# Kernel tuning notes

Hardware: AMD Instinct MI355X
Metric: run time of the kernel (lower is better)

## Reference

```python
import jax, jax.numpy as jnp
import numpy as np

N, D_IN = 16384, 1024
E, K = 16, 2
D_EMB, H_UNITS, D_HID = 128, 1024, 512


def setup_inputs() -> dict:
    key = jax.random.key(0)
    ks = jax.random.split(key, 10)
    s = lambda fan_in: 1.0 / np.sqrt(fan_in)
    return {
        "x": jax.random.normal(ks[0], (N, D_IN), jnp.float32),
        "Wr": jax.random.normal(ks[1], (D_IN, D_EMB), jnp.float32) * s(D_IN),
        "br": jnp.zeros((D_EMB,), jnp.float32),
        "expert_embeddings": jax.random.normal(ks[2], (E, D_EMB), jnp.float32) * s(D_EMB),
        "W1": jax.random.normal(ks[3], (E, D_IN, H_UNITS), jnp.float32) * s(D_IN),
        "b1": jnp.zeros((E, H_UNITS), jnp.float32),
        "W2": jax.random.normal(ks[4], (E, H_UNITS, H_UNITS // 2), jnp.float32) * s(H_UNITS),
        "b2": jnp.zeros((E, H_UNITS // 2), jnp.float32),
        "W3": jax.random.normal(ks[5], (E, H_UNITS // 2, D_HID), jnp.float32) * s(H_UNITS // 2),
        "b3": jnp.zeros((E, D_HID), jnp.float32),
    }


def reference(x, Wr, br, expert_embeddings, W1, b1, W2, b2, W3, b3):
    # Router: query per token [N, D_EMB]
    q = x @ Wr + br
    # Negative squared L2 distance to each expert embedding -> scores [N, E]
    d2 = jnp.sum(jnp.square(q[:, None, :] - expert_embeddings[None, :, :]), axis=-1)
    scores = -d2
    # Top-k gating (softmax over the k selected scores only)
    top_k_scores, top_k_idx = jax.lax.top_k(scores, K)        # [N, K]
    gates = jax.nn.softmax(top_k_scores, axis=-1)             # [N, K]
    # Dense all-expert MLP (as the original: every expert on every token)
    h1 = jax.nn.relu(jnp.einsum('nd,edh->enh', x, W1) + b1[:, None, :])   # [E,N,1024]
    h2 = jax.nn.relu(jnp.einsum('enh,ehm->enm', h1, W2) + b2[:, None, :]) # [E,N,512]
    eo = jnp.einsum('enm,emo->eno', h2, W3) + b3[:, None, :]              # [E,N,D_HID]
    eo_t = jnp.transpose(eo, (1, 0, 2))                                   # [N,E,D_HID]
    # Gather top-k expert outputs per token and combine with gates
    sel = jnp.take_along_axis(eo_t, top_k_idx[:, :, None], axis=1)        # [N,K,D_HID]
    combined = jnp.sum(sel * gates[:, :, None], axis=1)                   # [N,D_HID]
    return combined
```

## Files before the change

### kernel.cpp

```cpp
#include <hip/hip_runtime.h>

typedef unsigned short u16;
typedef __attribute__((ext_vector_type(8))) short short8;
typedef __attribute__((ext_vector_type(4))) float f32x4;

#define N_TOK 16384
#define DIN   1024
#define NE    16
#define DEMB  128
#define H1N   1024
#define H2N   512
#define DOUT  512
#define CAP   34816
#define MT    (CAP/128)
#define RBLK  1024

#define OFF_P      0ul
#define OFF_C      65536ul
#define OFF_CTRL   65792ul
#define OFF_E01    66048ul
#define OFF_G01    197120ul
#define OFF_GTOK   328192ul
#define OFF_GGATE  467456ul
#define OFF_BH     606720ul
#define OFF_BB     672256ul
#define OFF_W1T    737792ul
#define OFF_W2T    34292224ul
#define OFF_W3T    51069440ul
#define OFF_XBF    59458048ul
#define OFF_H1     93012480ul
#define OFF_H2     164315648ul

__device__ __forceinline__ u16 f2bf(float f) {
  union { float f; unsigned u; } v; v.f = f;
  unsigned r = v.u + 0x7fff + ((v.u >> 16) & 1);
  return (u16)(r >> 16);
}

__device__ __forceinline__ void async_copy16(const u16* g, u16* l) {
  __builtin_amdgcn_global_load_lds((const __attribute__((address_space(1))) unsigned*)g,
                                   (__attribute__((address_space(3))) unsigned*)l,
                                   16, 0, 0);
}

__global__ void router_prep(const float* __restrict__ Wr, const float* __restrict__ br,
                            const float* __restrict__ emb, float* __restrict__ P,
                            float* __restrict__ c) {
  int idx = blockIdx.x * 256 + threadIdx.x;
  int row = idx >> 4, e = idx & 15;
  float s = 0.f;
  for (int j = 0; j < DEMB; ++j) s += Wr[row * DEMB + j] * emb[e * DEMB + j];
  P[row * NE + e] = 2.f * s;
  if (idx < NE) {
    float cc = 0.f, n2 = 0.f;
    for (int j = 0; j < DEMB; ++j) {
      float ev = emb[idx * DEMB + j];
      cc += br[j] * ev;
      n2 += ev * ev;
    }
    c[idx] = 2.f * cc - n2;
  }
}

__global__ void __launch_bounds__(256) router_score(
    const float* __restrict__ x, const float* __restrict__ P,
    const float* __restrict__ c, int* __restrict__ e01,
    float* __restrict__ g01, int* __restrict__ bhist,
    u16* __restrict__ xbf) {
  __shared__ float xs[16384];
  __shared__ int lh[16];
  int wave = threadIdx.x >> 6, lane = threadIdx.x & 63;
  int e2 = lane & 7, kgl = lane >> 3;
  int tbase = blockIdx.x * 16 + wave * 4;
  float* xw = xs + wave * 4096;

  if (threadIdx.x < 16) lh[threadIdx.x] = 0;

  u16* xbrow = xbf + (size_t)tbase * DIN;
  #pragma unroll
  for (int t = 0; t < 4; ++t) {
    const float* src = x + (size_t)(tbase + t) * DIN;
    #pragma unroll
    for (int q = 0; q < 4; ++q) {
      int g = q * 256 + lane * 4;
      float4 v = *(const float4*)(src + g);
      *(float4*)(xw + t * 1024 + g) = v;
      ushort4 o;
      o.x = f2bf(v.x); o.y = f2bf(v.y); o.z = f2bf(v.z); o.w = f2bf(v.w);
      *(ushort4*)(xbrow + t * DIN + g) = o;
    }
  }
  __syncthreads();

  int te0 = 2 * e2, te1 = te0 + 1;
  float ce0 = c[te0], ce1 = c[te1];
  const float* Pb = P + te0;

  float acc0[4] = {0.f, 0.f, 0.f, 0.f};
  float acc1[4] = {0.f, 0.f, 0.f, 0.f};
  int cbase = kgl * 128;
  #pragma unroll 4
  for (int i = 0; i < 32; ++i) {
    int w = (kgl * 4 + i * 4) & 127;
    int idx = cbase + w;
    float2 pv0 = *(const float2*)(Pb + (size_t)(idx + 0) * NE);
    float2 pv1 = *(const float2*)(Pb + (size_t)(idx + 1) * NE);
    float2 pv2 = *(const float2*)(Pb + (size_t)(idx + 2) * NE);
    float2 pv3 = *(const float2*)(Pb + (size_t)(idx + 3) * NE);
    #pragma unroll
    for (int t = 0; t < 4; ++t) {
      float4 xv = *(const float4*)(xw + t * 1024 + idx);
      acc0[t] = fmaf(xv.x, pv0.x, acc0[t]); acc1[t] = fmaf(xv.x, pv0.y, acc1[t]);
      acc0[t] = fmaf(xv.y, pv1.x, acc0[t]); acc1[t] = fmaf(xv.y, pv1.y, acc1[t]);
      acc0[t] = fmaf(xv.z, pv2.x, acc0[t]); acc1[t] = fmaf(xv.z, pv2.y, acc1[t]);
      acc0[t] = fmaf(xv.w, pv3.x, acc0[t]); acc1[t] = fmaf(xv.w, pv3.y, acc1[t]);
    }
  }

  for (int t = 0; t < 4; ++t) {
    float s0 = acc0[t], s1 = acc1[t];
    #pragma unroll
    for (int off = 8; off <= 32; off <<= 1) {
      s0 += __shfl_xor(s0, off);
      s1 += __shfl_xor(s1, off);
    }
    s0 += ce0; s1 += ce1;
    float hi; int hidx;
    if (s0 >= s1) { hi = s0; hidx = te0; } else { hi = s1; hidx = te1; }
    float m1 = hi; int i1 = hidx;
    #pragma unroll
    for (int off = 1; off < 8; off <<= 1) {
      float so = __shfl_xor(m1, off); int io = __shfl_xor(i1, off);
      if (so > m1 || (so == m1 && io < i1)) { m1 = so; i1 = io; }
    }
    float c2; int c2i;
    if (i1 == te0)      { c2 = s1; c2i = te1; }
    else if (i1 == te1) { c2 = s0; c2i = te0; }
    else                { c2 = hi; c2i = hidx; }
    float m2 = c2; int i2 = c2i;
    #pragma unroll
    for (int off = 1; off < 8; off <<= 1) {
      float so = __shfl_xor(m2, off); int io = __shfl_xor(i2, off);
      if (so > m2 || (so == m2 && io < i2)) { m2 = so; i2 = io; }
    }
    if (lane == 0) {
      int tok = tbase + t;
      float ev = expf(m2 - m1);
      float inv = 1.f / (1.f + ev);
      e01[tok * 2 + 0] = i1; e01[tok * 2 + 1] = i2;
      g01[tok * 2 + 0] = inv; g01[tok * 2 + 1] = ev * inv;
      atomicAdd(&lh[i1], 1);
      atomicAdd(&lh[i2], 1);
    }
  }
  __syncthreads();
  if (threadIdx.x < 16) bhist[blockIdx.x * 16 + threadIdx.x] = lh[threadIdx.x];
}

__global__ void __launch_bounds__(1024) scan_offsets(
    const int* __restrict__ bhist, int* __restrict__ counts,
    int* __restrict__ poff, int* __restrict__ bbase, int* __restrict__ gtok) {
  int t = threadIdx.x;
  int e = t & 15, ch = t >> 4;
  int b0 = ch * 16;
  int s = 0;
  #pragma unroll
  for (int i = 0; i < 16; ++i) s += bhist[(b0 + i) * 16 + e];
  __shared__ int part[64][16];
  __shared__ int chbase[64][16];
  __shared__ int cnt[16];
  __shared__ int pof[16];
  part[ch][e] = s;
  __syncthreads();
  if (t < 16) {
    int run = 0;
    for (int c2 = 0; c2 < 64; ++c2) { chbase[c2][t] = run; run += part[c2][t]; }
    cnt[t] = run;
  }
  __syncthreads();
  if (t == 0) {
    int off = 0;
    for (int e2 = 0; e2 < NE; ++e2) {
      pof[e2] = off;
      poff[e2] = off;
      counts[e2] = cnt[e2];
      off += (cnt[e2] + 127) & ~127;
    }
    poff[NE] = off;
  }
  __syncthreads();
  int padc = ((cnt[e] + 127) & ~127) - cnt[e];
  int pbase = pof[e] + cnt[e];
  if (ch < padc) gtok[pbase + ch] = 0;
  if (ch + 64 < padc) gtok[pbase + ch + 64] = 0;

  int run = pof[e] + chbase[ch][e];
  #pragma unroll
  for (int i = 0; i < 16; ++i) {
    bbase[(b0 + i) * 16 + e] = run;
    run += bhist[(b0 + i) * 16 + e];
  }
}

__global__ void build_lists(const int* __restrict__ e01, const float* __restrict__ g01,
                            const int* __restrict__ bbase, int* __restrict__ gtok,
                            float* __restrict__ ggate) {
  __shared__ int pos[16];
  int tid = threadIdx.x;
  if (tid < 16) pos[tid] = bbase[blockIdx.x * 16 + tid];
  __syncthreads();
  if (tid < 16) {
    int t = blockIdx.x * 16 + tid;
    #pragma unroll
    for (int k = 0; k < 2; ++k) {
      int e = e01[t * 2 + k];
      int p = atomicAdd(&pos[e], 1);
      gtok[p] = t;
      ggate[p] = g01[t * 2 + k];
    }
  }
}

template<int K, int N>
__global__ void conv_w(const float* __restrict__ W, u16* __restrict__ WT) {
  __shared__ float tile[64][65];
  int e = blockIdx.z;
  int n0 = blockIdx.x * 64, k0 = blockIdx.y * 64;
  int tx = threadIdx.x & 63, ty = threadIdx.x >> 6;
  const float* Wb = W + (size_t)e * K * N;
  #pragma unroll
  for (int p = 0; p < 16; ++p) {
    int k = p * 4 + ty;
    tile[k][tx] = Wb[(size_t)(k0 + k) * N + n0 + tx];
  }
  __syncthreads();
  u16* WTb = WT + (size_t)e * N * K;
  #pragma unroll
  for (int p = 0; p < 16; ++p) {
    int n = p * 4 + ty;
    WTb[(size_t)(n0 + n) * K + k0 + tx] = f2bf(tile[tx][n]);
  }
}

template<int MODE, bool INDIR>
__global__ void __launch_bounds__(256)
gemm_moe(const u16* __restrict__ A, const u16* __restrict__ Ball,
         const float* __restrict__ bias, u16* __restrict__ Cb, float* __restrict__ outF,
         const int* __restrict__ poff, const int* __restrict__ counts,
         const int* __restrict__ gtok, const float* __restrict__ ggate,
         int K, int N, int nblk) {
  __shared__ u16 Asm[2][4096];
  __shared__ u16 Bsm[2][4096];

  int bid = blockIdx.x;
  int q = nblk >> 3, r = nblk & 7;
  int xcd = bid & 7, sidx = bid >> 3;
  int wg = (xcd < r ? xcd * (q + 1) : r * (q + 1) + (xcd - r) * q) + sidx;
  int NB = N >> 7;
  int rb = wg / NB, nb = wg - rb * NB;

  int row_base = rb * 128;
  if (row_base >= poff[NE]) return;
  int e = 0;
  while (row_base >= poff[e + 1]) ++e;

  int tid = threadIdx.x;
  int wave = tid >> 6, lane = tid & 63;
  int wm = wave >> 1, wn = wave & 1;
  int fr = lane & 15, kq = lane >> 4;
  int n_base = nb * 128;

  const u16* Brow = Ball + (size_t)e * N * K + (size_t)n_base * K;

  int rr0 = tid >> 2, rr1 = rr0 + 64;
  int ch8 = ((tid & 3) ^ ((rr0 >> 1) & 3)) * 8;
  const u16 *a0, *a1;
  if constexpr (INDIR) {
    a0 = A + (size_t)gtok[row_base + rr0] * K;
    a1 = A + (size_t)gtok[row_base + rr1] * K;
  } else {
    a0 = A + (size_t)(row_base + rr0) * K;
    a1 = A + (size_t)(row_base + rr1) * K;
  }
  const u16* b0 = Brow + (size_t)rr0 * K;
  const u16* b1 = Brow + (size_t)rr1 * K;

  f32x4 acc[4][4];
  #pragma unroll
  for (int m = 0; m < 4; ++m)
    #pragma unroll
    for (int n = 0; n < 4; ++n)
      acc[m][n] = (f32x4){0.f, 0.f, 0.f, 0.f};

  int swz = (fr >> 1) & 3;

  auto stage_tile = [&](int buf, int kt) {
    async_copy16(a0 + kt + ch8, &Asm[buf][tid * 8]);
    async_copy16(a1 + kt + ch8, &Asm[buf][(256 + tid) * 8]);
    async_copy16(b0 + kt + ch8, &Bsm[buf][tid * 8]);
    async_copy16(b1 + kt + ch8, &Bsm[buf][(256 + tid) * 8]);
  };

  stage_tile(0, 0);
  __syncthreads();

  int nstep = K >> 5;
  int cur = 0;
  for (int s = 0; s < nstep; ++s) {
    if (s + 1 < nstep) stage_tile(cur ^ 1, (s + 1) << 5);
    short8 av[4], bv[4];
    #pragma unroll
    for (int m = 0; m < 4; ++m)
      av[m] = *(const short8*)(&Asm[cur][((wm * 64 + m * 16 + fr) * 4 + (kq ^ swz)) * 8]);
    #pragma unroll
    for (int n = 0; n < 4; ++n)
      bv[n] = *(const short8*)(&Bsm[cur][((wn * 64 + n * 16 + fr) * 4 + (kq ^ swz)) * 8]);
    #pragma unroll
    for (int m = 0; m < 4; ++m)
      #pragma unroll
      for (int n = 0; n < 4; ++n)
        acc[m][n] = __builtin_amdgcn_mfma_f32_16x16x32_bf16(av[m], bv[n], acc[m][n], 0, 0, 0);
    __syncthreads();
    cur ^= 1;
  }

  int crow = (lane >> 4) * 4;
  int ccol = lane & 15;
  const float* be = bias + (size_t)e * N;
  if constexpr (MODE == 0) {
    #pragma unroll
    for (int m = 0; m < 4; ++m) {
      int gr0 = row_base + wm * 64 + m * 16 + crow;
      #pragma unroll
      for (int n = 0; n < 4; ++n) {
        int gc = n_base + wn * 64 + n * 16 + ccol;
        float bvs = be[gc];
        #pragma unroll
        for (int r2 = 0; r2 < 4; ++r2) {
          float v = acc[m][n][r2] + bvs;
          v = v > 0.f ? v : 0.f;
          Cb[(size_t)(gr0 + r2) * N + gc] = f2bf(v);
        }
      }
    }
  } else {
    int poe = poff[e], ce = counts[e];
    #pragma unroll
    for (int m = 0; m < 4; ++m) {
      int gr0 = row_base + wm * 64 + m * 16 + crow;
      int tk[4]; float gt[4]; bool vl[4];
      #pragma unroll
      for (int r2 = 0; r2 < 4; ++r2) {
        int gr = gr0 + r2;
        vl[r2] = (gr - poe) < ce;
        tk[r2] = vl[r2] ? gtok[gr] : 0;
        gt[r2] = vl[r2] ? ggate[gr] : 0.f;
      }
      #pragma unroll
      for (int n = 0; n < 4; ++n) {
        int gc = n_base + wn * 64 + n * 16 + ccol;
        float bvs = be[gc];
        #pragma unroll
        for (int r2 = 0; r2 < 4; ++r2) {
          if (vl[r2]) {
            float v = (acc[m][n][r2] + bvs) * gt[r2];
            atomicAdd(outF + (size_t)tk[r2] * N + gc, v);
          }
        }
      }
    }
  }
}

extern "C" void kernel_launch(void* const* d_in, const int* in_sizes, int n_in,
                              void* d_out, int out_size, void* d_ws, size_t ws_size,
                              hipStream_t stream) {
  const float* x   = (const float*)d_in[0];
  const float* Wr  = (const float*)d_in[1];
  const float* br  = (const float*)d_in[2];
  const float* emb = (const float*)d_in[3];
  const float* W1  = (const float*)d_in[4];
  const float* b1  = (const float*)d_in[5];
  const float* W2  = (const float*)d_in[6];
  const float* b2  = (const float*)d_in[7];
  const float* W3  = (const float*)d_in[8];
  const float* b3  = (const float*)d_in[9];
  float* out = (float*)d_out;
  char* ws = (char*)d_ws;

  float* P      = (float*)(ws + OFF_P);
  float* c      = (float*)(ws + OFF_C);
  int*   counts = (int*)(ws + OFF_CTRL);
  int*   poff   = (int*)(ws + OFF_CTRL + 128);
  int*   e01    = (int*)(ws + OFF_E01);
  float* g01    = (float*)(ws + OFF_G01);
  int*   gtok   = (int*)(ws + OFF_GTOK);
  float* ggate  = (float*)(ws + OFF_GGATE);
  int*   bhist  = (int*)(ws + OFF_BH);
  int*   bbase  = (int*)(ws + OFF_BB);
  u16*   W1T    = (u16*)(ws + OFF_W1T);
  u16*   W2T    = (u16*)(ws + OFF_W2T);
  u16*   W3T    = (u16*)(ws + OFF_W3T);
  u16*   xbf    = (u16*)(ws + OFF_XBF);
  u16*   h1     = (u16*)(ws + OFF_H1);
  u16*   h2     = (u16*)(ws + OFF_H2);

  hipMemsetAsync(d_out, 0, (size_t)N_TOK * DOUT * sizeof(float), stream);

  conv_w<DIN, H1N><<<dim3(H1N / 64, DIN / 64, NE), 256, 0, stream>>>(W1, W1T);
  conv_w<H1N, H2N><<<dim3(H2N / 64, H1N / 64, NE), 256, 0, stream>>>(W2, W2T);
  conv_w<H2N, DOUT><<<dim3(DOUT / 64, H2N / 64, NE), 256, 0, stream>>>(W3, W3T);

  router_prep<<<64, 256, 0, stream>>>(Wr, br, emb, P, c);
  router_score<<<RBLK, 256, 0, stream>>>(x, P, c, e01, g01, bhist, xbf);
  scan_offsets<<<1, 1024, 0, stream>>>(bhist, counts, poff, bbase, gtok);
  build_lists<<<RBLK, 64, 0, stream>>>(e01, g01, bbase, gtok, ggate);

  int nb1 = (H1N / 128) * MT;
  int nb2 = (H2N / 128) * MT;
  int nb3 = (DOUT / 128) * MT;
  gemm_moe<0, true><<<nb1, 256, 0, stream>>>(xbf, W1T, b1, h1, nullptr,
                                             poff, counts, gtok, nullptr, DIN, H1N, nb1);
  gemm_moe<0, false><<<nb2, 256, 0, stream>>>(h1, W2T, b2, h2, nullptr,
                                              poff, counts, nullptr, nullptr, H1N, H2N, nb2);
  gemm_moe<1, false><<<nb3, 256, 0, stream>>>(h2, W3T, b3, nullptr, out,
                                              poff, counts, gtok, ggate, H2N, DOUT, nb3);
}
```

Before: 343.1 us.

## Replace atomic scatter-add in final GEMM with dense store plus combine kernel

The final expert GEMM now writes plain fp32 rows into a slot-ordered buffer that reuses the h1 workspace region, and does not scatter gated results into the output with atomicAdd. build_lists records each token's two slot positions, and a new combine_out kernel reads both rows and computes the gated sum per token. This removes the output memset and the float atomic traffic. In exchange it adds an extra write and read of the expert output (about 34816x512 floats) and one more kernel launch. The epilogue is now selected with MODE 2, which the visible else branch handles.

Measured after the change: 291.8 us. 1.18x faster.

```diff
diff --git a/kernel.cpp b/kernel.cpp
--- a/kernel.cpp
+++ b/kernel.cpp
@@ -22,14 +22,16 @@
 #define OFF_G01    197120ul
 #define OFF_GTOK   328192ul
 #define OFF_GGATE  467456ul
-#define OFF_BH     606720ul
-#define OFF_BB     672256ul
-#define OFF_W1T    737792ul
-#define OFF_W2T    34292224ul
-#define OFF_W3T    51069440ul
-#define OFF_XBF    59458048ul
-#define OFF_H1     93012480ul
-#define OFF_H2     164315648ul
+#define OFF_TSLOT  606720ul
+#define OFF_BH     737792ul
+#define OFF_BB     803328ul
+#define OFF_W1T    868864ul
+#define OFF_W2T    34423296ul
+#define OFF_W3T    51200512ul
+#define OFF_XBF    59589120ul
+#define OFF_H1     93143552ul
+#define OFF_H2     164446720ul
+#define OFF_EO     OFF_H1
 
 __device__ __forceinline__ u16 f2bf(float f) {
   union { float f; unsigned u; } v; v.f = f;
@@ -204,7 +206,7 @@
 
 __global__ void build_lists(const int* __restrict__ e01, const float* __restrict__ g01,
                             const int* __restrict__ bbase, int* __restrict__ gtok,
-                            float* __restrict__ ggate) {
+                            float* __restrict__ ggate, int* __restrict__ tslot) {
   __shared__ int pos[16];
   int tid = threadIdx.x;
   if (tid < 16) pos[tid] = bbase[blockIdx.x * 16 + tid];
@@ -217,6 +219,7 @@
       int p = atomicAdd(&pos[e], 1);
       gtok[p] = t;
       ggate[p] = g01[t * 2 + k];
+      tslot[t * 2 + k] = p;
     }
   }
 }
@@ -344,31 +347,41 @@
       }
     }
   } else {
-    int poe = poff[e], ce = counts[e];
     #pragma unroll
     for (int m = 0; m < 4; ++m) {
       int gr0 = row_base + wm * 64 + m * 16 + crow;
-      int tk[4]; float gt[4]; bool vl[4];
-      #pragma unroll
-      for (int r2 = 0; r2 < 4; ++r2) {
-        int gr = gr0 + r2;
-        vl[r2] = (gr - poe) < ce;
-        tk[r2] = vl[r2] ? gtok[gr] : 0;
-        gt[r2] = vl[r2] ? ggate[gr] : 0.f;
-      }
       #pragma unroll
       for (int n = 0; n < 4; ++n) {
         int gc = n_base + wn * 64 + n * 16 + ccol;
         float bvs = be[gc];
         #pragma unroll
-        for (int r2 = 0; r2 < 4; ++r2) {
-          if (vl[r2]) {
-            float v = (acc[m][n][r2] + bvs) * gt[r2];
-            atomicAdd(outF + (size_t)tk[r2] * N + gc, v);
-          }
-        }
+        for (int r2 = 0; r2 < 4; ++r2)
+          outF[(size_t)(gr0 + r2) * N + gc] = acc[m][n][r2] + bvs;
       }
     }
+  }
+}
+
+__global__ void __launch_bounds__(256) combine_out(
+    const float* __restrict__ eo, const int* __restrict__ tslot,
+    const float* __restrict__ g01, float* __restrict__ out) {
+  int wave = threadIdx.x >> 6, lane = threadIdx.x & 63;
+  int tok = blockIdx.x * 4 + wave;
+  int s0 = tslot[tok * 2 + 0], s1 = tslot[tok * 2 + 1];
+  float g0 = g01[tok * 2 + 0], g1 = g01[tok * 2 + 1];
+  const float* r0 = eo + (size_t)s0 * DOUT + lane * 8;
+  const float* r1 = eo + (size_t)s1 * DOUT + lane * 8;
+  float* o = out + (size_t)tok * DOUT + lane * 8;
+  #pragma unroll
+  for (int j = 0; j < 2; ++j) {
+    float4 v0 = ((const float4*)r0)[j];
+    float4 v1 = ((const float4*)r1)[j];
+    float4 ov;
+    ov.x = g0 * v0.x + g1 * v1.x;
+    ov.y = g0 * v0.y + g1 * v1.y;
+    ov.z = g0 * v0.z + g1 * v1.z;
+    ov.w = g0 * v0.w + g1 * v1.w;
+    ((float4*)o)[j] = ov;
   }
 }
 
@@ -396,6 +409,7 @@
   float* g01    = (float*)(ws + OFF_G01);
   int*   gtok   = (int*)(ws + OFF_GTOK);
   float* ggate  = (float*)(ws + OFF_GGATE);
+  int*   tslot  = (int*)(ws + OFF_TSLOT);
   int*   bhist  = (int*)(ws + OFF_BH);
   int*   bbase  = (int*)(ws + OFF_BB);
   u16*   W1T    = (u16*)(ws + OFF_W1T);
@@ -404,8 +418,7 @@
   u16*   xbf    = (u16*)(ws + OFF_XBF);
   u16*   h1     = (u16*)(ws + OFF_H1);
   u16*   h2     = (u16*)(ws + OFF_H2);
-
-  hipMemsetAsync(d_out, 0, (size_t)N_TOK * DOUT * sizeof(float), stream);
+  float* eo     = (float*)(ws + OFF_EO);
 
   conv_w<DIN, H1N><<<dim3(H1N / 64, DIN / 64, NE), 256, 0, stream>>>(W1, W1T);
   conv_w<H1N, H2N><<<dim3(H2N / 64, H1N / 64, NE), 256, 0, stream>>>(W2, W2T);
@@ -414,7 +427,7 @@
   router_prep<<<64, 256, 0, stream>>>(Wr, br, emb, P, c);
   router_score<<<RBLK, 256, 0, stream>>>(x, P, c, e01, g01, bhist, xbf);
   scan_offsets<<<1, 1024, 0, stream>>>(bhist, counts, poff, bbase, gtok);
-  build_lists<<<RBLK, 64, 0, stream>>>(e01, g01, bbase, gtok, ggate);
+  build_lists<<<RBLK, 64, 0, stream>>>(e01, g01, bbase, gtok, ggate, tslot);
 
   int nb1 = (H1N / 128) * MT;
   int nb2 = (H2N / 128) * MT;
@@ -423,6 +436,7 @@
                                              poff, counts, gtok, nullptr, DIN, H1N, nb1);
   gemm_moe<0, false><<<nb2, 256, 0, stream>>>(h1, W2T, b2, h2, nullptr,
                                               poff, counts, nullptr, nullptr, H1N, H2N, nb2);
-  gemm_moe<1, false><<<nb3, 256, 0, stream>>>(h2, W3T, b3, nullptr, out,
-                                              poff, counts, gtok, ggate, H2N, DOUT, nb3);
-}
+  gemm_moe<2, false><<<nb3, 256, 0, stream>>>(h2, W3T, b3, nullptr, eo,
+                                              poff, counts, nullptr, nullptr, H2N, DOUT, nb3);
+  combine_out<<<N_TOK / 4, 256, 0, stream>>>(eo, tslot, g01, out);
+}
```
